# Performance work log

Measured on AMD Instinct MI355X. Metric: run time of the kernel, lower is better.

## Reference

```python
import jax, jax.numpy as jnp
import numpy as np

M, N, H, C = 32, 1024, 64, 10  # samples, nodes(==feature dim), hidden, classes
SLOPE = 0.2


def setup_inputs() -> dict:
    key = jax.random.key(0)
    ks = jax.random.split(key, 6)
    features = jax.random.normal(ks[0], (M, N, N), jnp.float32)           # [M, N, D], D == N
    weights = jax.random.uniform(ks[1], (M, N, N), jnp.float32)           # nonneg adjacency weights
    std = (2.0 / (1.0 + SLOPE ** 2) / N) ** 0.5                            # kaiming_normal for leaky_relu
    w_gnn0 = jax.random.normal(ks[2], (N, H), jnp.float32) * std
    w_gnn1 = jax.random.normal(ks[3], (N, H), jnp.float32) * std
    w_gnn2 = jax.random.normal(ks[4], (N, H), jnp.float32) * std
    fc_w = jax.random.normal(ks[5], (H, C), jnp.float32) * (1.0 / H ** 0.5)
    fc_b = jnp.zeros((C,), jnp.float32)
    return {
        "features": features,
        "weights": weights,
        "w_gnn0": w_gnn0,
        "w_gnn1": w_gnn1,
        "w_gnn2": w_gnn2,
        "fc_w": fc_w,
        "fc_b": fc_b,
        "view_flag": 0,
    }


def _forward(features, weights, w_gnn0, w_gnn1, w_gnn2, fc_w, fc_b, view_flag):
    Wg = (w_gnn0, w_gnn1, w_gnn2)[view_flag]  # static selection
    _, Nn, _ = features.shape
    Cc = fc_b.shape[0]
    eye = jnp.eye(Nn, dtype=features.dtype)
    rows = jnp.arange(Nn)

    def structural_enhancement(W, p):
        # Literal torch semantics: max_id is always 0 (scores_list[i] is 0-dim),
        # so rows i < p get column-0 entry set to 1 where > 0. Score/cos-sim
        # suppression never affects outputs (scores_list is discarded).
        col0 = W[:, 0]
        new_col0 = jnp.where((rows < p) & (col0 > 0), jnp.asarray(1.0, W.dtype), col0)
        return W.at[:, 0].set(new_col0)

    def per_sample(X, W0):
        XW = X @ Wg  # [N, H]; X and Wg are loop-invariant
        feat_s = jnp.zeros((Wg.shape[1],), X.dtype)
        sr_s = jnp.zeros((Cc,), X.dtype)
        b_s = jnp.zeros((Cc,), X.dtype)
        u_s = jnp.asarray(0.0, X.dtype)
        u0 = jnp.asarray(999.0, X.dtype)
        done = jnp.asarray(False)
        W = W0
        for t in range(1, 9):  # while-loop is bounded: break guaranteed at 5*t >= 40
            adjp = 0.5 * structural_enhancement(W, 5 * t) + eye  # [N, N]
            h = adjp @ XW                                         # [N, H]
            h = jnp.where(h >= 0, h, SLOPE * h)                   # leaky_relu (dropout p=0 / eval)
            feat = h.mean(axis=0)                                 # global avg pool over nodes -> [H]
            sr = jax.nn.softplus(feat @ fc_w + fc_b)              # [C]
            S = sr.sum() + Cc
            u = Cc / S
            brk = (u >= u0) | (5 * t >= 40)
            store = jnp.logical_and(~done, ~brk)
            W = jnp.where(store, adjp, W)
            u0 = jnp.where(store, u, u0)
            feat_s = jnp.where(store, feat, feat_s)
            sr_s = jnp.where(store, sr, sr_s)
            b_s = jnp.where(store, sr / S, b_s)
            u_s = jnp.where(store, u, u_s)
            done = jnp.logical_or(done, brk)
        return feat_s, W, sr_s, b_s, u_s

    return jax.vmap(per_sample)(features, weights)


def reference(features, weights, w_gnn0, w_gnn1, w_gnn2, fc_w, fc_b, view_flag):
    # returns (aft_feat [M,H], weights [M,N,N], single_results [M,C], bb [M,C], uu [M])
    return _forward(features, weights, w_gnn0, w_gnn1, w_gnn2, fc_w, fc_b, view_flag)
```

## Files before the change

### kernel.cpp

```cpp
#include <hip/hip_runtime.h>
#include <math.h>

#define MS 32
#define NN 1024
#define HH 64
#define CC 10
#define SLOPEF 0.2f

typedef __attribute__((ext_vector_type(8))) short bf16x8;
typedef __attribute__((ext_vector_type(4))) float f32x4;

__device__ __forceinline__ void split2(float v, unsigned short& hi, unsigned short& lo) {
    unsigned u = __builtin_bit_cast(unsigned, v);
    hi = (unsigned short)(u >> 16);
    float hf = __builtin_bit_cast(float, u & 0xFFFF0000u);
    float l = v - hf;
    lo = (unsigned short)(__builtin_bit_cast(unsigned, l) >> 16);
}

template <int FUSED>
__global__ __launch_bounds__(256, 2) void gemm_bf16x3(
    const float* __restrict__ A, long aStride,
    const float* __restrict__ B0, const float* __restrict__ B1,
    const float* __restrict__ B2, const int* __restrict__ viewFlag,
    long bStride, float* __restrict__ Cmat, long cStride)
{
    __shared__ __align__(16) unsigned short Ahi[64 * 64];
    __shared__ __align__(16) unsigned short Alo[64 * 64];
    __shared__ __align__(16) unsigned short Bhi[64 * 64];
    __shared__ __align__(16) unsigned short Blo[64 * 64];
    __shared__ float x0s[64];
    __shared__ float red2[4][8][64];

    const int m = blockIdx.y;
    const int row0 = blockIdx.x * 64;
    const float* A_m = A + (long)m * aStride + (long)row0 * NN;
    const float* B_m;
    if (bStride == 0) {
        int vf = viewFlag[0];
        B_m = (vf == 0) ? B0 : (vf == 1 ? B1 : B2);
    } else {
        B_m = B0 + (long)m * bStride;
    }

    const int tid = threadIdx.x;
    const int w   = tid >> 6;
    const int l   = tid & 63;
    const int l15 = l & 15;
    const int lg  = l >> 4;

    const int bcol = tid & 63;
    const int bk0  = (tid >> 6) * 16;

    f32x4 acc[4] = {};

    for (int kc = 0; kc < NN; kc += 64) {
        float4 av[4];
        #pragma unroll
        for (int q = 0; q < 4; ++q) {
            int lin = q * 256 + tid;
            int r   = lin >> 4;
            int c4  = (lin & 15) << 2;
            av[q] = *reinterpret_cast<const float4*>(A_m + (long)r * NN + kc + c4);
        }
        float bv[16];
        #pragma unroll
        for (int i = 0; i < 16; ++i)
            bv[i] = B_m[(long)(kc + bk0 + i) * HH + bcol];

        #pragma unroll
        for (int q = 0; q < 4; ++q) {
            int lin = q * 256 + tid;
            int r   = lin >> 4;
            int c4  = (lin & 15) << 2;
            ushort4 h, lw;
            split2(av[q].x, h.x, lw.x);
            split2(av[q].y, h.y, lw.y);
            split2(av[q].z, h.z, lw.z);
            split2(av[q].w, h.w, lw.w);
            int byte = (r * 128 + c4 * 2) ^ ((r & 7) << 4);
            *reinterpret_cast<ushort4*>((char*)Ahi + byte) = h;
            *reinterpret_cast<ushort4*>((char*)Alo + byte) = lw;
        }
        {
            unsigned short bh[16], bl[16];
            #pragma unroll
            for (int i = 0; i < 16; ++i) split2(bv[i], bh[i], bl[i]);
            int base = bcol * 128 + bk0 * 2;
            int sw   = (bcol & 7) << 4;
            #pragma unroll
            for (int half = 0; half < 2; ++half) {
                ushort4 h0, l0, h1, l1;
                h0.x = bh[half*8+0]; h0.y = bh[half*8+1]; h0.z = bh[half*8+2]; h0.w = bh[half*8+3];
                h1.x = bh[half*8+4]; h1.y = bh[half*8+5]; h1.z = bh[half*8+6]; h1.w = bh[half*8+7];
                l0.x = bl[half*8+0]; l0.y = bl[half*8+1]; l0.z = bl[half*8+2]; l0.w = bl[half*8+3];
                l1.x = bl[half*8+4]; l1.y = bl[half*8+5]; l1.z = bl[half*8+6]; l1.w = bl[half*8+7];
                int byte = (base + half * 16) ^ sw;
                *reinterpret_cast<ushort4*>((char*)Bhi + byte)     = h0;
                *reinterpret_cast<ushort4*>((char*)Bhi + byte + 8) = h1;
                *reinterpret_cast<ushort4*>((char*)Blo + byte)     = l0;
                *reinterpret_cast<ushort4*>((char*)Blo + byte + 8) = l1;
            }
        }
        __syncthreads();

        #pragma unroll
        for (int s = 0; s < 2; ++s) {
            int arow  = w * 16 + l15;
            int abyte = (arow * 128 + s * 64 + lg * 16) ^ ((arow & 7) << 4);
            bf16x8 ah = *reinterpret_cast<bf16x8*>((char*)Ahi + abyte);
            bf16x8 al = *reinterpret_cast<bf16x8*>((char*)Alo + abyte);
            #pragma unroll
            for (int fc = 0; fc < 4; ++fc) {
                int col   = fc * 16 + l15;
                int bbyte = (col * 128 + s * 64 + lg * 16) ^ ((col & 7) << 4);
                bf16x8 bh8 = *reinterpret_cast<bf16x8*>((char*)Bhi + bbyte);
                bf16x8 bl8 = *reinterpret_cast<bf16x8*>((char*)Blo + bbyte);
                acc[fc] = __builtin_amdgcn_mfma_f32_16x16x32_bf16(ah, bh8, acc[fc], 0, 0, 0);
                acc[fc] = __builtin_amdgcn_mfma_f32_16x16x32_bf16(ah, bl8, acc[fc], 0, 0, 0);
                acc[fc] = __builtin_amdgcn_mfma_f32_16x16x32_bf16(al, bh8, acc[fc], 0, 0, 0);
            }
        }
        __syncthreads();
    }

    if constexpr (!FUSED) {
        float* C_m = Cmat + (long)m * cStride + (long)row0 * HH;
        #pragma unroll
        for (int fc = 0; fc < 4; ++fc) {
            #pragma unroll
            for (int r = 0; r < 4; ++r) {
                int row = w * 16 + lg * 4 + r;
                int col = fc * 16 + l15;
                C_m[(long)row * HH + col] = acc[fc][r];
            }
        }
    } else {
        if (tid < 64) x0s[tid] = B_m[tid];
        __syncthreads();

        int grows[4]; float v[4], bc[4];
        #pragma unroll
        for (int r = 0; r < 4; ++r) {
            int lrow = w * 16 + lg * 4 + r;
            grows[r] = row0 + lrow;
            v[r] = A_m[(long)lrow * NN];
            bc[r] = 0.0f;
        }
        float xwv[4][4];
        #pragma unroll
        for (int fc = 0; fc < 4; ++fc) {
            int col = fc * 16 + l15;
            #pragma unroll
            for (int r = 0; r < 4; ++r)
                xwv[fc][r] = B_m[(long)grows[r] * HH + col];
        }

        float alpha = 1.0f, gamma = 0.0f;
        #pragma unroll
        for (int t = 1; t <= 8; ++t) {
            #pragma unroll
            for (int r = 0; r < 4; ++r) {
                float c = (grows[r] < 5 * t && v[r] > 0.0f) ? (1.0f - v[r]) : 0.0f;
                bc[r] = 0.5f * (bc[r] + c);
                v[r]  = 0.5f * (v[r] + c) + (grows[r] == 0 ? 1.0f : 0.0f);
            }
            alpha *= 0.5f;
            gamma = 0.5f * gamma + 1.0f;
            #pragma unroll
            for (int fc = 0; fc < 4; ++fc) {
                float x0c = x0s[fc * 16 + l15];
                float s = 0.0f;
                #pragma unroll
                for (int r = 0; r < 4; ++r) {
                    float y = alpha * acc[fc][r] + bc[r] * x0c + gamma * xwv[fc][r];
                    s += (y >= 0.0f) ? y : SLOPEF * y;
                }
                s += __shfl_xor(s, 16);
                s += __shfl_xor(s, 32);
                if (l < 16) red2[w][t - 1][fc * 16 + l] = s;
            }
        }
        __syncthreads();
        if (tid < 512) {
            int t8 = tid >> 6, col = tid & 63;
            float p = red2[0][t8][col] + red2[1][t8][col] +
                      red2[2][t8][col] + red2[3][t8][col];
            Cmat[(((long)m * 16 + blockIdx.x) * 8 + t8) * 64 + col] = p;
        }
    }
}

__global__ __launch_bounds__(512) void decide_kernel(
    const float* __restrict__ partials,
    const float* __restrict__ weights,
    const float* __restrict__ fc_w,
    const float* __restrict__ fc_b,
    float* __restrict__ col0k,
    int* __restrict__ k_arr,
    float* __restrict__ out_feat,
    float* __restrict__ out_sr,
    float* __restrict__ out_b,
    float* __restrict__ out_u)
{
    __shared__ float feat[8][64];
    __shared__ float sr_all[8][CC];
    __shared__ float Ss[8], us[8];
    __shared__ int ksh;

    const int m = blockIdx.x;
    const int tid = threadIdx.x;

    {
        int t8 = tid >> 6, col = tid & 63;
        float s = 0.0f;
        for (int bx = 0; bx < 16; ++bx)
            s += partials[(((long)m * 16 + bx) * 8 + t8) * 64 + col];
        feat[t8][col] = s * (1.0f / NN);
    }
    __syncthreads();

    if (tid < 80) {
        int t8 = tid / 10, c = tid % 10;
        float a = fc_b[c];
        for (int h = 0; h < HH; ++h) a += feat[t8][h] * fc_w[h * CC + c];
        sr_all[t8][c] = log1pf(expf(-fabsf(a))) + fmaxf(a, 0.0f);
    }
    __syncthreads();

    if (tid < 8) {
        float S = (float)CC;
        for (int c = 0; c < CC; ++c) S += sr_all[tid][c];
        Ss[tid] = S;
        us[tid] = (float)CC / S;
    }
    __syncthreads();

    if (tid == 0) {
        float u0 = 999.0f; int k = 1;
        for (int tt = 1; tt <= 8; ++tt) {
            float u = us[tt - 1];
            int brk = (u >= u0) || (tt == 8);
            if (!brk) { k = tt; u0 = u; } else break;
        }
        ksh = k;
        k_arr[m] = k;
        out_u[m] = us[k - 1];
    }
    __syncthreads();

    const int k = ksh;
    if (tid < 64) out_feat[m * HH + tid] = feat[k - 1][tid];
    if (tid < CC) {
        out_sr[m * CC + tid] = sr_all[k - 1][tid];
        out_b[m * CC + tid]  = sr_all[k - 1][tid] / Ss[k - 1];
    }
    for (int i = tid; i < NN; i += 512) {
        float v = weights[(long)m * NN * NN + (long)i * NN];
        for (int s = 1; s <= k; ++s) {
            float c = (i < 5 * s && v > 0.0f) ? (1.0f - v) : 0.0f;
            v = 0.5f * (v + c) + (i == 0 ? 1.0f : 0.0f);
        }
        col0k[m * NN + i] = v;
    }
}

__global__ __launch_bounds__(256) void finalize_W(
    const float* __restrict__ W0, const float* __restrict__ col0k,
    const int* __restrict__ k_arr, float* __restrict__ outW)
{
    const long n4 = (long)MS * NN * NN / 4;
    long i4 = (long)blockIdx.x * blockDim.x + threadIdx.x;
    if (i4 >= n4) return;
    long e = i4 * 4;
    int m = (int)(e >> 20);
    int i = (int)((e >> 10) & 1023);
    int j = (int)(e & 1023);
    int k = k_arr[m];
    float scale = 1.0f / (float)(1 << k);
    float diagadd = 2.0f * (1.0f - scale);

    float4 wv = reinterpret_cast<const float4*>(W0)[i4];
    float v0 = scale * wv.x + ((i == j + 0) ? diagadd : 0.0f);
    float v1 = scale * wv.y + ((i == j + 1) ? diagadd : 0.0f);
    float v2 = scale * wv.z + ((i == j + 2) ? diagadd : 0.0f);
    float v3 = scale * wv.w + ((i == j + 3) ? diagadd : 0.0f);
    if (j == 0) v0 = col0k[m * NN + i];
    float4 o = make_float4(v0, v1, v2, v3);
    reinterpret_cast<float4*>(outW)[i4] = o;
}

extern "C" void kernel_launch(void* const* d_in, const int* in_sizes, int n_in,
                              void* d_out, int out_size, void* d_ws, size_t ws_size,
                              hipStream_t stream)
{
    const float* features = (const float*)d_in[0];
    const float* weights  = (const float*)d_in[1];
    const float* w_gnn0   = (const float*)d_in[2];
    const float* w_gnn1   = (const float*)d_in[3];
    const float* w_gnn2   = (const float*)d_in[4];
    const float* fc_w     = (const float*)d_in[5];
    const float* fc_b     = (const float*)d_in[6];
    const int*   viewFlag = (const int*)d_in[7];

    float* out = (float*)d_out;
    float* out_feat = out;
    float* outW     = out + (long)MS * HH;
    float* out_sr   = outW + (long)MS * NN * NN;
    float* out_b    = out_sr + MS * CC;
    float* out_u    = out_b + MS * CC;

    float* wsf      = (float*)d_ws;
    float* XW       = wsf;
    float* partials = XW + (long)MS * NN * HH;
    float* col0k    = partials + (long)MS * 16 * 8 * 64;
    int*   k_arr    = (int*)(col0k + (long)MS * NN);

    dim3 gemmGrid(NN / 64, MS);
    gemm_bf16x3<0><<<gemmGrid, 256, 0, stream>>>(features, (long)NN * NN,
                                                 w_gnn0, w_gnn1, w_gnn2, viewFlag,
                                                 0L, XW, (long)NN * HH);
    gemm_bf16x3<1><<<gemmGrid, 256, 0, stream>>>(weights, (long)NN * NN,
                                                 XW, XW, XW, viewFlag,
                                                 (long)NN * HH, partials, 0L);
    decide_kernel<<<MS, 512, 0, stream>>>(partials, weights, fc_w, fc_b,
                                          col0k, k_arr,
                                          out_feat, out_sr, out_b, out_u);
    long n4 = (long)MS * NN * NN / 4;
    int blocks = (int)((n4 + 255) / 256);
    finalize_W<<<blocks, 256, 0, stream>>>(weights, col0k, k_arr, outW);
}
```

Baseline: 133.7 us.

## Pre-split B operands into transposed bf16 hi/lo and feed MFMA from registers

```diff
diff --git a/kernel.cpp b/kernel.cpp
--- a/kernel.cpp
+++ b/kernel.cpp
@@ -18,114 +18,141 @@
     lo = (unsigned short)(__builtin_bit_cast(unsigned, l) >> 16);
 }
 
+__device__ __forceinline__ void transpose_split_body(
+    const float* __restrict__ src,
+    int k0,
+    unsigned short* __restrict__ dh,
+    unsigned short* __restrict__ dl)
+{
+    __shared__ float tile[64][65];
+    const int t = threadIdx.x;
+    #pragma unroll
+    for (int q = 0; q < 4; ++q) {
+        int lin = q * 256 + t;
+        int r = lin >> 4;
+        int c4 = (lin & 15) << 2;
+        float4 v = *reinterpret_cast<const float4*>(src + (long)r * HH + c4);
+        tile[r][c4 + 0] = v.x; tile[r][c4 + 1] = v.y;
+        tile[r][c4 + 2] = v.z; tile[r][c4 + 3] = v.w;
+    }
+    __syncthreads();
+    const int col = t >> 2;
+    const int seg = t & 3;
+    unsigned short h8[16], l8[16];
+    #pragma unroll
+    for (int j = 0; j < 16; ++j)
+        split2(tile[seg * 16 + j][col], h8[j], l8[j]);
+    long off = (long)col * NN + k0 + seg * 16;
+    *reinterpret_cast<float4*>(dh + off)     = *reinterpret_cast<float4*>(h8);
+    *reinterpret_cast<float4*>(dh + off + 8) = *reinterpret_cast<float4*>(h8 + 8);
+    *reinterpret_cast<float4*>(dl + off)     = *reinterpret_cast<float4*>(l8);
+    *reinterpret_cast<float4*>(dl + off + 8) = *reinterpret_cast<float4*>(l8 + 8);
+}
+
+__global__ __launch_bounds__(256) void split_B_sel(
+    const float* __restrict__ B0, const float* __restrict__ B1,
+    const float* __restrict__ B2, const int* __restrict__ flag,
+    unsigned short* __restrict__ dh, unsigned short* __restrict__ dl)
+{
+    int vf = flag[0];
+    const float* B = (vf == 0) ? B0 : (vf == 1 ? B1 : B2);
+    int k0 = blockIdx.x * 64;
+    transpose_split_body(B + (long)k0 * HH, k0, dh, dl);
+}
+
+__global__ __launch_bounds__(256) void split_B_xw(
+    const float* __restrict__ XWf,
+    unsigned short* __restrict__ dh, unsigned short* __restrict__ dl)
+{
+    int m = blockIdx.y;
+    int k0 = blockIdx.x * 64;
+    transpose_split_body(XWf + (long)m * NN * HH + (long)k0 * HH, k0,
+                         dh + (long)m * HH * NN, dl + (long)m * HH * NN);
+}
+
 template <int FUSED>
-__global__ __launch_bounds__(256, 2) void gemm_bf16x3(
+__global__ __launch_bounds__(256, 2) void gemm_frag(
     const float* __restrict__ A, long aStride,
-    const float* __restrict__ B0, const float* __restrict__ B1,
-    const float* __restrict__ B2, const int* __restrict__ viewFlag,
-    long bStride, float* __restrict__ Cmat, long cStride)
-{
-    __shared__ __align__(16) unsigned short Ahi[64 * 64];
-    __shared__ __align__(16) unsigned short Alo[64 * 64];
-    __shared__ __align__(16) unsigned short Bhi[64 * 64];
-    __shared__ __align__(16) unsigned short Blo[64 * 64];
-    __shared__ float x0s[64];
-    __shared__ float red2[4][8][64];
-
+    const unsigned short* __restrict__ Bh, const unsigned short* __restrict__ Bl,
+    long bStrideH,
+    const float* __restrict__ XWf,
+    float* __restrict__ Cmat)
+{
     const int m = blockIdx.y;
     const int row0 = blockIdx.x * 64;
-    const float* A_m = A + (long)m * aStride + (long)row0 * NN;
-    const float* B_m;
-    if (bStride == 0) {
-        int vf = viewFlag[0];
-        B_m = (vf == 0) ? B0 : (vf == 1 ? B1 : B2);
-    } else {
-        B_m = B0 + (long)m * bStride;
-    }
-
     const int tid = threadIdx.x;
     const int w   = tid >> 6;
     const int l   = tid & 63;
     const int l15 = l & 15;
     const int lg  = l >> 4;
 
-    const int bcol = tid & 63;
-    const int bk0  = (tid >> 6) * 16;
+    const float* Ar = A + (long)m * aStride + (long)(row0 + w * 16 + l15) * NN;
+    const unsigned short* bh_base = Bh + (bStrideH ? (long)m * bStrideH : 0L);
+    const unsigned short* bl_base = Bl + (bStrideH ? (long)m * bStrideH : 0L);
 
     f32x4 acc[4] = {};
 
-    for (int kc = 0; kc < NN; kc += 64) {
-        float4 av[4];
-        #pragma unroll
-        for (int q = 0; q < 4; ++q) {
-            int lin = q * 256 + tid;
-            int r   = lin >> 4;
-            int c4  = (lin & 15) << 2;
-            av[q] = *reinterpret_cast<const float4*>(A_m + (long)r * NN + kc + c4);
-        }
-        float bv[16];
-        #pragma unroll
-        for (int i = 0; i < 16; ++i)
-            bv[i] = B_m[(long)(kc + bk0 + i) * HH + bcol];
-
-        #pragma unroll
-        for (int q = 0; q < 4; ++q) {
-            int lin = q * 256 + tid;
-            int r   = lin >> 4;
-            int c4  = (lin & 15) << 2;
-            ushort4 h, lw;
-            split2(av[q].x, h.x, lw.x);
-            split2(av[q].y, h.y, lw.y);
-            split2(av[q].z, h.z, lw.z);
-            split2(av[q].w, h.w, lw.w);
-            int byte = (r * 128 + c4 * 2) ^ ((r & 7) << 4);
-            *reinterpret_cast<ushort4*>((char*)Ahi + byte) = h;
-            *reinterpret_cast<ushort4*>((char*)Alo + byte) = lw;
-        }
-        {
-            unsigned short bh[16], bl[16];
-            #pragma unroll
-            for (int i = 0; i < 16; ++i) split2(bv[i], bh[i], bl[i]);
-            int base = bcol * 128 + bk0 * 2;
-            int sw   = (bcol & 7) << 4;
-            #pragma unroll
-            for (int half = 0; half < 2; ++half) {
-                ushort4 h0, l0, h1, l1;
-                h0.x = bh[half*8+0]; h0.y = bh[half*8+1]; h0.z = bh[half*8+2]; h0.w = bh[half*8+3];
-                h1.x = bh[half*8+4]; h1.y = bh[half*8+5]; h1.z = bh[half*8+6]; h1.w = bh[half*8+7];
-                l0.x = bl[half*8+0]; l0.y = bl[half*8+1]; l0.z = bl[half*8+2]; l0.w = bl[half*8+3];
-                l1.x = bl[half*8+4]; l1.y = bl[half*8+5]; l1.z = bl[half*8+6]; l1.w = bl[half*8+7];
-                int byte = (base + half * 16) ^ sw;
-                *reinterpret_cast<ushort4*>((char*)Bhi + byte)     = h0;
-                *reinterpret_cast<ushort4*>((char*)Bhi + byte + 8) = h1;
-                *reinterpret_cast<ushort4*>((char*)Blo + byte)     = l0;
-                *reinterpret_cast<ushort4*>((char*)Blo + byte + 8) = l1;
-            }
-        }
-        __syncthreads();
-
-        #pragma unroll
-        for (int s = 0; s < 2; ++s) {
-            int arow  = w * 16 + l15;
-            int abyte = (arow * 128 + s * 64 + lg * 16) ^ ((arow & 7) << 4);
-            bf16x8 ah = *reinterpret_cast<bf16x8*>((char*)Ahi + abyte);
-            bf16x8 al = *reinterpret_cast<bf16x8*>((char*)Alo + abyte);
+    int ko = lg * 8;
+    f32x4 a0, a1;
+    if (FUSED) {
+        a0 = *reinterpret_cast<const f32x4*>(Ar + ko);
+        a1 = *reinterpret_cast<const f32x4*>(Ar + ko + 4);
+    } else {
+        a0 = __builtin_nontemporal_load(reinterpret_cast<const f32x4*>(Ar + ko));
+        a1 = __builtin_nontemporal_load(reinterpret_cast<const f32x4*>(Ar + ko + 4));
+    }
+    bf16x8 pbh[4], pbl[4];
+    #pragma unroll
+    for (int fc = 0; fc < 4; ++fc) {
+        long boff = (long)(fc * 16 + l15) * NN + ko;
+        pbh[fc] = *reinterpret_cast<const bf16x8*>(bh_base + boff);
+        pbl[fc] = *reinterpret_cast<const bf16x8*>(bl_base + boff);
+    }
+
+    for (int ks = 0; ks < 32; ++ks) {
+        f32x4 ca0 = a0, ca1 = a1;
+        bf16x8 cbh0 = pbh[0], cbh1 = pbh[1], cbh2 = pbh[2], cbh3 = pbh[3];
+        bf16x8 cbl0 = pbl[0], cbl1 = pbl[1], cbl2 = pbl[2], cbl3 = pbl[3];
+        if (ks < 31) {
+            int ko2 = (ks + 1) * 32 + lg * 8;
+            if (FUSED) {
+                a0 = *reinterpret_cast<const f32x4*>(Ar + ko2);
+                a1 = *reinterpret_cast<const f32x4*>(Ar + ko2 + 4);
+            } else {
+                a0 = __builtin_nontemporal_load(reinterpret_cast<const f32x4*>(Ar + ko2));
+                a1 = __builtin_nontemporal_load(reinterpret_cast<const f32x4*>(Ar + ko2 + 4));
+            }
             #pragma unroll
             for (int fc = 0; fc < 4; ++fc) {
-                int col   = fc * 16 + l15;
-                int bbyte = (col * 128 + s * 64 + lg * 16) ^ ((col & 7) << 4);
-                bf16x8 bh8 = *reinterpret_cast<bf16x8*>((char*)Bhi + bbyte);
-                bf16x8 bl8 = *reinterpret_cast<bf16x8*>((char*)Blo + bbyte);
-                acc[fc] = __builtin_amdgcn_mfma_f32_16x16x32_bf16(ah, bh8, acc[fc], 0, 0, 0);
-                acc[fc] = __builtin_amdgcn_mfma_f32_16x16x32_bf16(ah, bl8, acc[fc], 0, 0, 0);
-                acc[fc] = __builtin_amdgcn_mfma_f32_16x16x32_bf16(al, bh8, acc[fc], 0, 0, 0);
-            }
-        }
-        __syncthreads();
+                long boff = (long)(fc * 16 + l15) * NN + ko2;
+                pbh[fc] = *reinterpret_cast<const bf16x8*>(bh_base + boff);
+                pbl[fc] = *reinterpret_cast<const bf16x8*>(bl_base + boff);
+            }
+        }
+        unsigned short ah[8], al[8];
+        split2(ca0.x, ah[0], al[0]); split2(ca0.y, ah[1], al[1]);
+        split2(ca0.z, ah[2], al[2]); split2(ca0.w, ah[3], al[3]);
+        split2(ca1.x, ah[4], al[4]); split2(ca1.y, ah[5], al[5]);
+        split2(ca1.z, ah[6], al[6]); split2(ca1.w, ah[7], al[7]);
+        bf16x8 ahv = *reinterpret_cast<bf16x8*>(ah);
+        bf16x8 alv = *reinterpret_cast<bf16x8*>(al);
+
+        acc[0] = __builtin_amdgcn_mfma_f32_16x16x32_bf16(ahv, cbh0, acc[0], 0, 0, 0);
+        acc[0] = __builtin_amdgcn_mfma_f32_16x16x32_bf16(ahv, cbl0, acc[0], 0, 0, 0);
+        acc[0] = __builtin_amdgcn_mfma_f32_16x16x32_bf16(alv, cbh0, acc[0], 0, 0, 0);
+        acc[1] = __builtin_amdgcn_mfma_f32_16x16x32_bf16(ahv, cbh1, acc[1], 0, 0, 0);
+        acc[1] = __builtin_amdgcn_mfma_f32_16x16x32_bf16(ahv, cbl1, acc[1], 0, 0, 0);
+        acc[1] = __builtin_amdgcn_mfma_f32_16x16x32_bf16(alv, cbh1, acc[1], 0, 0, 0);
+        acc[2] = __builtin_amdgcn_mfma_f32_16x16x32_bf16(ahv, cbh2, acc[2], 0, 0, 0);
+        acc[2] = __builtin_amdgcn_mfma_f32_16x16x32_bf16(ahv, cbl2, acc[2], 0, 0, 0);
+        acc[2] = __builtin_amdgcn_mfma_f32_16x16x32_bf16(alv, cbh2, acc[2], 0, 0, 0);
+        acc[3] = __builtin_amdgcn_mfma_f32_16x16x32_bf16(ahv, cbh3, acc[3], 0, 0, 0);
+        acc[3] = __builtin_amdgcn_mfma_f32_16x16x32_bf16(ahv, cbl3, acc[3], 0, 0, 0);
+        acc[3] = __builtin_amdgcn_mfma_f32_16x16x32_bf16(alv, cbh3, acc[3], 0, 0, 0);
     }
 
     if constexpr (!FUSED) {
-        float* C_m = Cmat + (long)m * cStride + (long)row0 * HH;
+        float* C_m = Cmat + (long)m * NN * HH + (long)row0 * HH;
         #pragma unroll
         for (int fc = 0; fc < 4; ++fc) {
             #pragma unroll
@@ -136,7 +163,10 @@
             }
         }
     } else {
-        if (tid < 64) x0s[tid] = B_m[tid];
+        __shared__ float x0s[64];
+        __shared__ float red2[4][8][64];
+        const float* XWm = XWf + (long)m * NN * HH;
+        if (tid < 64) x0s[tid] = XWm[tid];
         __syncthreads();
 
         int grows[4]; float v[4], bc[4];
@@ -144,7 +174,7 @@
         for (int r = 0; r < 4; ++r) {
             int lrow = w * 16 + lg * 4 + r;
             grows[r] = row0 + lrow;
-            v[r] = A_m[(long)lrow * NN];
+            v[r] = A[(long)m * aStride + (long)grows[r] * NN];
             bc[r] = 0.0f;
         }
         float xwv[4][4];
@@ -153,7 +183,7 @@
             int col = fc * 16 + l15;
             #pragma unroll
             for (int r = 0; r < 4; ++r)
-                xwv[fc][r] = B_m[(long)grows[r] * HH + col];
+                xwv[fc][r] = XWm[(long)grows[r] * HH + col];
         }
 
         float alpha = 1.0f, gamma = 0.0f;
@@ -270,24 +300,25 @@
     const int* __restrict__ k_arr, float* __restrict__ outW)
 {
     const long n4 = (long)MS * NN * NN / 4;
-    long i4 = (long)blockIdx.x * blockDim.x + threadIdx.x;
-    if (i4 >= n4) return;
-    long e = i4 * 4;
-    int m = (int)(e >> 20);
-    int i = (int)((e >> 10) & 1023);
-    int j = (int)(e & 1023);
-    int k = k_arr[m];
-    float scale = 1.0f / (float)(1 << k);
-    float diagadd = 2.0f * (1.0f - scale);
-
-    float4 wv = reinterpret_cast<const float4*>(W0)[i4];
-    float v0 = scale * wv.x + ((i == j + 0) ? diagadd : 0.0f);
-    float v1 = scale * wv.y + ((i == j + 1) ? diagadd : 0.0f);
-    float v2 = scale * wv.z + ((i == j + 2) ? diagadd : 0.0f);
-    float v3 = scale * wv.w + ((i == j + 3) ? diagadd : 0.0f);
-    if (j == 0) v0 = col0k[m * NN + i];
-    float4 o = make_float4(v0, v1, v2, v3);
-    reinterpret_cast<float4*>(outW)[i4] = o;
+    const long stride = (long)gridDim.x * 256;
+    for (long i4 = (long)blockIdx.x * 256 + threadIdx.x; i4 < n4; i4 += stride) {
+        long e = i4 * 4;
+        int m = (int)(e >> 20);
+        int i = (int)((e >> 10) & 1023);
+        int j = (int)(e & 1023);
+        int k = k_arr[m];
+        float scale = 1.0f / (float)(1 << k);
+        float diagadd = 2.0f * (1.0f - scale);
+
+        f32x4 wv = reinterpret_cast<const f32x4*>(W0)[i4];
+        float v0 = scale * wv.x + ((i == j + 0) ? diagadd : 0.0f);
+        float v1 = scale * wv.y + ((i == j + 1) ? diagadd : 0.0f);
+        float v2 = scale * wv.z + ((i == j + 2) ? diagadd : 0.0f);
+        float v3 = scale * wv.w + ((i == j + 3) ? diagadd : 0.0f);
+        if (j == 0) v0 = col0k[m * NN + i];
+        f32x4 o = {v0, v1, v2, v3};
+        __builtin_nontemporal_store(o, reinterpret_cast<f32x4*>(outW) + i4);
+    }
 }
 
 extern "C" void kernel_launch(void* const* d_in, const int* in_sizes, int n_in,
@@ -310,23 +341,25 @@
     float* out_b    = out_sr + MS * CC;
     float* out_u    = out_b + MS * CC;
 
-    float* wsf      = (float*)d_ws;
-    float* XW       = wsf;
-    float* partials = XW + (long)MS * NN * HH;
-    float* col0k    = partials + (long)MS * 16 * 8 * 64;
-    int*   k_arr    = (int*)(col0k + (long)MS * NN);
-
+    float* wsf = (float*)d_ws;
+    float* XWf            = wsf;
+    unsigned short* XWh   = (unsigned short*)(XWf + (long)MS * NN * HH);
+    unsigned short* XWl   = XWh + (long)MS * HH * NN;
+    unsigned short* Wgh   = XWl + (long)MS * HH * NN;
+    unsigned short* Wgl   = Wgh + (long)HH * NN;
+    float* partials       = (float*)(Wgl + (long)HH * NN);
+    float* col0k          = partials + (long)MS * 16 * 8 * 64;
+    int*   k_arr          = (int*)(col0k + (long)MS * NN);
+
+    split_B_sel<<<16, 256, 0, stream>>>(w_gnn0, w_gnn1, w_gnn2, viewFlag, Wgh, Wgl);
     dim3 gemmGrid(NN / 64, MS);
-    gemm_bf16x3<0><<<gemmGrid, 256, 0, stream>>>(features, (long)NN * NN,
-                                                 w_gnn0, w_gnn1, w_gnn2, viewFlag,
-                                                 0L, XW, (long)NN * HH);
-    gemm_bf16x3<1><<<gemmGrid, 256, 0, stream>>>(weights, (long)NN * NN,
-                                                 XW, XW, XW, viewFlag,
-                                                 (long)NN * HH, partials, 0L);
+    gemm_frag<0><<<gemmGrid, 256, 0, stream>>>(features, (long)NN * NN,
+                                               Wgh, Wgl, 0L, nullptr, XWf);
+    split_B_xw<<<dim3(16, MS), 256, 0, stream>>>(XWf, XWh, XWl);
+    gemm_frag<1><<<gemmGrid, 256, 0, stream>>>(weights, (long)NN * NN,
+                                               XWh, XWl, (long)HH * NN, XWf, partials);
     decide_kernel<<<MS, 512, 0, stream>>>(partials, weights, fc_w, fc_b,
                                           col0k, k_arr,
                                           out_feat, out_sr, out_b, out_u);
-    long n4 = (long)MS * NN * NN / 4;
-    int blocks = (int)((n4 + 255) / 256);
-    finalize_W<<<blocks, 256, 0, stream>>>(weights, col0k, k_arr, outW);
-}
+    finalize_W<<<2048, 256, 0, stream>>>(weights, col0k, k_arr, outW);
+}
```

Result: slower. 223.5 us (+67.2%).
